# Optimization experiments

Measured on AMD Instinct MI355X. Metric: run time of the kernel, lower is better.

Reference implementation:

```python
import jax, jax.numpy as jnp
import numpy as np

D_MODEL = 1024
N_HEADS = 16
TREE_DEPTH = 5
B, T = 2, 1024


def setup_inputs() -> dict:
    key = jax.random.key(0)
    k1, k2, k3, k4 = jax.random.split(key, 4)
    sc = 1.0 / np.sqrt(D_MODEL)
    return {
        "x": jax.random.normal(k1, (B, T, D_MODEL), dtype=jnp.float32),
        "Wp": jax.random.normal(k2, (D_MODEL, N_HEADS * TREE_DEPTH), dtype=jnp.float32) * sc,
        "bp": jnp.zeros((N_HEADS * TREE_DEPTH,), dtype=jnp.float32),
        "Wv": jax.random.normal(k3, (D_MODEL, D_MODEL), dtype=jnp.float32) * sc,
        "Wo": jax.random.normal(k4, (D_MODEL, D_MODEL), dtype=jnp.float32) * sc,
    }


def reference(x, Wp, bp, Wv, Wo):
    Bc, Tc, d = x.shape
    H, Dt = N_HEADS, TREE_DEPTH
    dh = d // H
    # tree paths: (B, H, T, Dt)
    paths = jax.nn.sigmoid(x @ Wp + bp).reshape(Bc, Tc, H, Dt).transpose(0, 2, 1, 3)
    pq = paths[:, :, :, None, :]  # (B,H,T,1,Dt)
    pk = paths[:, :, None, :, :]  # (B,H,1,T,Dt)
    agree = pq * pk + (1.0 - pq) * (1.0 - pk)  # (B,H,T,T,Dt)
    sim = jnp.cumprod(agree, axis=-1).sum(axis=-1) / Dt  # (B,H,T,T)
    # causal mask (strict upper triangle -> -inf)
    causal_mask = jnp.triu(jnp.ones((Tc, Tc), dtype=bool), k=1)
    sim = jnp.where(causal_mask[None, None], -jnp.inf, sim)
    attn = jax.nn.softmax(sim, axis=-1)
    V = (x @ Wv).reshape(Bc, Tc, H, dh).transpose(0, 2, 1, 3)  # (B,H,T,dh)
    ctx = jnp.einsum("bhqk,bhkd->bhqd", attn, V)
    ctx = ctx.transpose(0, 2, 1, 3).reshape(Bc, Tc, d)
    return ctx @ Wo
```

## Files before the change

kernel.cpp:

```cpp
#include <hip/hip_runtime.h>
#include <hip/hip_bf16.h>

#define B_SZ 2
#define T_SEQ 1024
#define D_MODEL 1024
#define N_HEADS 16
#define TREE_DEPTH 5
#define DH 64

typedef __attribute__((ext_vector_type(8))) short short8;
typedef __attribute__((ext_vector_type(4))) float f32x4;

__device__ __forceinline__ ushort f2bf(float f) {
    uint32_t u = __float_as_uint(f);
    u += 0x7FFFu + ((u >> 16) & 1u);
    return (ushort)(u >> 16);
}

__device__ __forceinline__ void gll16(const void* g, void* l) {
    __builtin_amdgcn_global_load_lds(
        (const __attribute__((address_space(1))) void*)g,
        (__attribute__((address_space(3))) void*)l, 16, 0, 0);
}

__global__ __launch_bounds__(256) void prologue(
    const float* __restrict__ x, const float* __restrict__ Wv,
    const float* __restrict__ Wo, const float* __restrict__ Wp,
    ushort* __restrict__ xb, ushort* __restrict__ Wvt,
    ushort* __restrict__ Wot, ushort* __restrict__ Wpt)
{
    __shared__ __align__(16) char sm[20480];
    const int bid = blockIdx.x, tid = threadIdx.x;
    if (bid < 1024) {
        const int i = (bid * 256 + tid) * 8;
        const float4 a = *(const float4*)(x + i);
        const float4 b = *(const float4*)(x + i + 4);
        ushort o[8] = {f2bf(a.x), f2bf(a.y), f2bf(a.z), f2bf(a.w),
                       f2bf(b.x), f2bf(b.y), f2bf(b.z), f2bf(b.w)};
        *(uint4*)(xb + i) = *(const uint4*)o;
    } else if (bid < 3072) {
        const int t = bid - 1024;
        const float* W = (t < 1024) ? Wv : Wo;
        ushort* Wt = (t < 1024) ? Wvt : Wot;
        const int ti = t & 1023;
        const int n0 = (ti & 31) * 32, k0 = (ti >> 5) * 32;
        float (*tile)[33] = (float(*)[33])sm;
        const int tx = tid & 31, ty = tid >> 5;
        #pragma unroll
        for (int i = 0; i < 4; ++i)
            tile[ty + i * 8][tx] = W[(size_t)(k0 + ty + i * 8) * 1024 + n0 + tx];
        __syncthreads();
        #pragma unroll
        for (int i = 0; i < 4; ++i)
            Wt[(size_t)(n0 + ty + i * 8) * 1024 + k0 + tx] = f2bf(tile[tx][ty + i * 8]);
    } else {
        float* tile = (float*)sm;
        const int k0 = (bid - 3072) * 64;
        #pragma unroll
        for (int j = 0; j < 20; ++j) {
            const int i = tid + j * 256;
            tile[i] = Wp[(size_t)k0 * 80 + i];
        }
        __syncthreads();
        #pragma unroll
        for (int j = 0; j < 20; ++j) {
            const int o = tid + j * 256;
            const int n = o >> 6, k = o & 63;
            Wpt[(size_t)n * 1024 + k0 + k] = f2bf(tile[k * 80 + n]);
        }
    }
}

template <bool OUT_BF16>
__device__ __forceinline__ void gemm_body(
    const ushort* __restrict__ A, const ushort* __restrict__ Bt,
    void* __restrict__ Cv, int N, int K, int bx, int by,
    ushort* As, ushort* Bs)
{
    const int tid = threadIdx.x;
    const int lane = tid & 63;
    const int w = tid >> 6;
    const int wm = w & 1, wn = w >> 1;
    const int rowBase = by * 128;
    const int colBase = bx * 64;

    const int srow = lane & 15;
    const int sk = (lane >> 4) * 8;

    const ushort* gA0 = A + (size_t)(rowBase + 2 * w * 16 + srow) * K + sk;
    const ushort* gA1 = gA0 + (size_t)16 * K;
    const ushort* gB  = Bt + (size_t)(colBase + w * 16 + srow) * K + sk;
    ushort* dA0 = As + (2 * w) * 512;
    ushort* dA1 = As + (2 * w + 1) * 512;
    ushort* dB  = Bs + w * 512;

    f32x4 acc[4][2];
    #pragma unroll
    for (int i = 0; i < 4; ++i) {
        acc[i][0] = (f32x4)0.0f;
        acc[i][1] = (f32x4)0.0f;
    }

    for (int it = 0; it < K / 32; ++it) {
        __syncthreads();
        gll16(gA0 + it * 32, dA0);
        gll16(gA1 + it * 32, dA1);
        gll16(gB  + it * 32, dB);
        __syncthreads();
        short8 af[4], bf[2];
        #pragma unroll
        for (int j = 0; j < 4; ++j)
            af[j] = *(const short8*)(As + (wm * 4 + j) * 512 + lane * 8);
        #pragma unroll
        for (int j = 0; j < 2; ++j)
            bf[j] = *(const short8*)(Bs + (wn * 2 + j) * 512 + lane * 8);
        #pragma unroll
        for (int i = 0; i < 4; ++i)
            #pragma unroll
            for (int j = 0; j < 2; ++j)
                acc[i][j] = __builtin_amdgcn_mfma_f32_16x16x32_bf16(
                    af[i], bf[j], acc[i][j], 0, 0, 0);
    }

    const int cq = lane >> 4, cl = lane & 15;
    #pragma unroll
    for (int i = 0; i < 4; ++i)
        #pragma unroll
        for (int j = 0; j < 2; ++j) {
            const int col = colBase + wn * 32 + j * 16 + cl;
            #pragma unroll
            for (int r = 0; r < 4; ++r) {
                const int row = rowBase + wm * 64 + i * 16 + cq * 4 + r;
                if (OUT_BF16)
                    ((ushort*)Cv)[(size_t)row * N + col] = f2bf(acc[i][j][r]);
                else
                    ((float*)Cv)[(size_t)row * N + col] = acc[i][j][r];
            }
        }
}

__device__ __forceinline__ void phi_body(
    const ushort* __restrict__ xb, const ushort* __restrict__ Wpt,
    const float* __restrict__ bp, ushort* __restrict__ Phi,
    int blk, float* red, float* p_s)
{
    const int tid = threadIdx.x;
    const int lane = tid & 63, w = tid >> 6;
    const int quad = lane >> 4, m16 = lane & 15;
    const int row0 = blk * 16;

    f32x4 acc[5];
    #pragma unroll
    for (int nb = 0; nb < 5; ++nb) acc[nb] = (f32x4)0.0f;

    const ushort* ap = xb + (size_t)(row0 + m16) * 1024 + w * 256 + quad * 8;
    const ushort* bpz = Wpt + (size_t)m16 * 1024 + w * 256 + quad * 8;
    #pragma unroll
    for (int it = 0; it < 8; ++it) {
        const short8 af = *(const short8*)(ap + it * 32);
        #pragma unroll
        for (int nb = 0; nb < 5; ++nb) {
            const short8 bf = *(const short8*)(bpz + (size_t)nb * 16 * 1024 + it * 32);
            acc[nb] = __builtin_amdgcn_mfma_f32_16x16x32_bf16(af, bf, acc[nb], 0, 0, 0);
        }
    }
    #pragma unroll
    for (int nb = 0; nb < 5; ++nb)
        #pragma unroll
        for (int r = 0; r < 4; ++r)
            red[(w * 16 + quad * 4 + r) * 80 + nb * 16 + m16] = acc[nb][r];
    __syncthreads();
    #pragma unroll
    for (int j = 0; j < 5; ++j) {
        const int i = tid + j * 256;
        const int rr = i / 80, cc = i - rr * 80;
        const float v = red[(0 * 16 + rr) * 80 + cc] + red[(1 * 16 + rr) * 80 + cc] +
                        red[(2 * 16 + rr) * 80 + cc] + red[(3 * 16 + rr) * 80 + cc] + bp[cc];
        p_s[rr * 80 + cc] = 1.0f / (1.0f + __expf(-v));
    }
    __syncthreads();
    #pragma unroll
    for (int j = 0; j < 8; ++j) {
        const int c = tid + j * 256;
        const int rr = c >> 7, rem = c & 127;
        const int h = rem >> 3, f8 = (rem & 7) * 8;
        const float* pr = &p_s[rr * 80 + h * 5];
        ushort o[8];
        #pragma unroll
        for (int e = 0; e < 8; ++e) {
            const int f = f8 + e;
            float val = 0.0f;
            if (f < 62) {
                int d, off;
                if (f < 2)       { d = 1; off = 0; }
                else if (f < 6)  { d = 2; off = 2; }
                else if (f < 14) { d = 3; off = 6; }
                else if (f < 30) { d = 4; off = 14; }
                else             { d = 5; off = 30; }
                const int e2 = f - off;
                float prod = 1.0f;
                for (int jj = 1; jj <= d; ++jj) {
                    const float p = pr[jj - 1];
                    prod *= ((e2 >> (d - jj)) & 1) ? (1.0f - p) : p;
                }
                val = prod;
            }
            o[e] = f2bf(val);
        }
        const int grow = row0 + rr;
        const int b = grow >> 10, t = grow & 1023;
        *(uint4*)(Phi + ((size_t)(b * 16 + h) * 1024 + t) * 64 + f8) =
            *(const uint4*)o;
    }
}

__global__ __launch_bounds__(256) void mid_kernel(
    const ushort* __restrict__ xb, const ushort* __restrict__ Wvt,
    const ushort* __restrict__ Wpt, const float* __restrict__ bp,
    ushort* __restrict__ Vt, ushort* __restrict__ Phi)
{
    __shared__ __align__(16) char sm[25600];
    if (blockIdx.x < 256) {
        ushort* As = (ushort*)sm;
        ushort* Bs = As + 128 * 32;
        gemm_body<true>(Wvt, xb, Vt, 2048, 1024,
                        blockIdx.x & 31, blockIdx.x >> 5, As, Bs);
    } else {
        float* red = (float*)sm;
        float* p_s = (float*)(sm + 20480);
        phi_body(xb, Wpt, bp, Phi, blockIdx.x - 256, red, p_s);
    }
}

__global__ __launch_bounds__(256) void gemm_out(
    const ushort* __restrict__ ctxb, const ushort* __restrict__ Wot,
    float* __restrict__ out)
{
    __shared__ __align__(16) ushort sm[128 * 32 + 64 * 32];
    gemm_body<false>(ctxb, Wot, out, 1024, 1024,
                     blockIdx.x, blockIdx.y, sm, sm + 128 * 32);
}

__global__ __launch_bounds__(256) void attn_mfma(
    const ushort* __restrict__ Phi, const ushort* __restrict__ Vt,
    ushort* __restrict__ ctxb)
{
    const int qt = 15 - blockIdx.x;
    const int bh = blockIdx.y;
    const int b = bh >> 4, h = bh & 15;
    const int tid = threadIdx.x;
    const int lane = tid & 63;
    const int w = tid >> 6;
    const int quad = lane >> 4, m16 = lane & 15;

    __shared__ ushort K_s[4096];
    __shared__ ushort V_s[4096];
    __shared__ ushort W_s[4096];

    const int qrow = qt * 64 + w * 16 + m16;
    const ushort* qbase = Phi + ((size_t)bh * 1024 + qrow) * 64 + quad * 8;
    const short8 qf0 = *(const short8*)qbase;
    const short8 qf1 = *(const short8*)(qbase + 32);

    f32x4 cacc[4];
    #pragma unroll
    for (int nb = 0; nb < 4; ++nb) cacc[nb] = (f32x4)0.0f;
    float den[4] = {0.f, 0.f, 0.f, 0.f};

    const int r0 = tid >> 3;
    const int c8 = (tid & 7) * 8;
    const int ks_st = c8 >> 5, kc_st = (c8 >> 3) & 3;

    for (int kt = 0; kt <= qt; ++kt) {
        __syncthreads();
        #pragma unroll
        for (int i = 0; i < 2; ++i) {
            const int r = r0 + i * 32;
            const int dst = ((r >> 4) * 2 + ks_st) * 512 + (kc_st * 16 + (r & 15)) * 8;
            *(uint4*)(K_s + dst) =
                *(const uint4*)(Phi + ((size_t)bh * 1024 + kt * 64 + r) * 64 + c8);
            *(uint4*)(V_s + dst) =
                *(const uint4*)(Vt + (size_t)(h * 64 + r) * (B_SZ * T_SEQ) +
                                b * 1024 + kt * 64 + c8);
        }
        __syncthreads();

        #pragma unroll
        for (int nb = 0; nb < 4; ++nb) {
            const short8 kf0 = *(const short8*)(K_s + (nb * 2 + 0) * 512 + lane * 8);
            const short8 kf1 = *(const short8*)(K_s + (nb * 2 + 1) * 512 + lane * 8);
            f32x4 s = (f32x4)0.0f;
            s = __builtin_amdgcn_mfma_f32_16x16x32_bf16(qf0, kf0, s, 0, 0, 0);
            s = __builtin_amdgcn_mfma_f32_16x16x32_bf16(qf1, kf1, s, 0, 0, 0);
            const int key = nb * 16 + m16;
            const int kglob = kt * 64 + key;
            const int qg0 = qt * 64 + w * 16 + quad * 4;
            const int wbase = (w * 2 + (key >> 5)) * 512 + (((key >> 3) & 3) * 16) * 8 +
                              (quad * 4) * 8 + (key & 7);
            #pragma unroll
            for (int r = 0; r < 4; ++r) {
                float wgt = 0.0f;
                if (kglob <= qg0 + r) wgt = __expf(s[r] * 0.2f);
                den[r] += wgt;
                W_s[wbase + r * 8] = f2bf(wgt);
            }
        }
        __syncthreads();

        const short8 wf0 = *(const short8*)(W_s + (w * 2 + 0) * 512 + lane * 8);
        const short8 wf1 = *(const short8*)(W_s + (w * 2 + 1) * 512 + lane * 8);
        #pragma unroll
        for (int nb = 0; nb < 4; ++nb) {
            const short8 vf0 = *(const short8*)(V_s + (nb * 2 + 0) * 512 + lane * 8);
            const short8 vf1 = *(const short8*)(V_s + (nb * 2 + 1) * 512 + lane * 8);
            cacc[nb] = __builtin_amdgcn_mfma_f32_16x16x32_bf16(wf0, vf0, cacc[nb], 0, 0, 0);
            cacc[nb] = __builtin_amdgcn_mfma_f32_16x16x32_bf16(wf1, vf1, cacc[nb], 0, 0, 0);
        }
    }

    #pragma unroll
    for (int r = 0; r < 4; ++r) {
        den[r] += __shfl_xor(den[r], 1);
        den[r] += __shfl_xor(den[r], 2);
        den[r] += __shfl_xor(den[r], 4);
        den[r] += __shfl_xor(den[r], 8);
        den[r] = 1.0f / den[r];
    }

    #pragma unroll
    for (int nb = 0; nb < 4; ++nb) {
        const int dim = h * 64 + nb * 16 + m16;
        #pragma unroll
        for (int r = 0; r < 4; ++r) {
            const int token = qt * 64 + w * 16 + quad * 4 + r;
            ctxb[(size_t)(b * 1024 + token) * D_MODEL + dim] = f2bf(cacc[nb][r] * den[r]);
        }
    }
}

extern "C" void kernel_launch(void* const* d_in, const int* in_sizes, int n_in,
                              void* d_out, int out_size, void* d_ws, size_t ws_size,
                              hipStream_t stream)
{
    const float* x  = (const float*)d_in[0];
    const float* Wp = (const float*)d_in[1];
    const float* bp = (const float*)d_in[2];
    const float* Wv = (const float*)d_in[3];
    const float* Wo = (const float*)d_in[4];
    float* out = (float*)d_out;

    char* ws = (char*)d_ws;
    ushort* xb   = (ushort*)(ws);
    ushort* Wvt  = (ushort*)(ws + (4u  << 20));
    ushort* Wot  = (ushort*)(ws + (6u  << 20));
    ushort* Phi  = (ushort*)(ws + (8u  << 20));
    ushort* Vt   = (ushort*)(ws + (12u << 20));
    ushort* ctxb = (ushort*)(ws + (16u << 20));
    ushort* Wpt  = (ushort*)(ws + (20u << 20));

    prologue<<<3088, 256, 0, stream>>>(x, Wv, Wo, Wp, xb, Wvt, Wot, Wpt);
    mid_kernel<<<384, 256, 0, stream>>>(xb, Wvt, Wpt, bp, Vt, Phi);
    attn_mfma<<<dim3(16, 32), 256, 0, stream>>>(Phi, Vt, ctxb);
    gemm_out<<<dim3(16, 16), 256, 0, stream>>>(ctxb, Wot, out);
}
```

Before: 160.1 us.

## Double-buffer GEMM and attention tiles with async global-to-LDS loads, shrink GEMM tiles

The shared GEMM body moves from a 128x64 tile with a K-step of 32 to a 64x64 tile with a K-step of 64. It double-buffers LDS so the next tile's global_load_lds is issued before the current tile is computed, and the grids double to 512 blocks for the V projection and 16x32 for the output projection. The attention kernel now streams K and V through double-buffered LDS with async direct-to-LDS loads instead of register staging. It computes transposed scores so each lane packs its weights into one 8-byte LDS write, and reduces the softmax denominator through shared memory. The intent is to hide global load latency, cut barriers per tile and raise occupancy and block count, at the cost of more LDS per block and less reuse per tile.

Result: faster. 151.5 us (-5.4%).

```diff
diff --git a/kernel.cpp b/kernel.cpp
--- a/kernel.cpp
+++ b/kernel.cpp
@@ -81,56 +81,66 @@
     const int lane = tid & 63;
     const int w = tid >> 6;
     const int wm = w & 1, wn = w >> 1;
-    const int rowBase = by * 128;
+    const int rowBase = by * 64;
     const int colBase = bx * 64;
 
     const int srow = lane & 15;
     const int sk = (lane >> 4) * 8;
 
-    const ushort* gA0 = A + (size_t)(rowBase + 2 * w * 16 + srow) * K + sk;
-    const ushort* gA1 = gA0 + (size_t)16 * K;
-    const ushort* gB  = Bt + (size_t)(colBase + w * 16 + srow) * K + sk;
-    ushort* dA0 = As + (2 * w) * 512;
-    ushort* dA1 = As + (2 * w + 1) * 512;
-    ushort* dB  = Bs + w * 512;
-
-    f32x4 acc[4][2];
-    #pragma unroll
-    for (int i = 0; i < 4; ++i) {
+    const ushort* gA = A + (size_t)(rowBase + w * 16 + srow) * K + sk;
+    const ushort* gB = Bt + (size_t)(colBase + w * 16 + srow) * K + sk;
+
+    f32x4 acc[2][2];
+    #pragma unroll
+    for (int i = 0; i < 2; ++i) {
         acc[i][0] = (f32x4)0.0f;
         acc[i][1] = (f32x4)0.0f;
     }
 
-    for (int it = 0; it < K / 32; ++it) {
-        __syncthreads();
-        gll16(gA0 + it * 32, dA0);
-        gll16(gA1 + it * 32, dA1);
-        gll16(gB  + it * 32, dB);
-        __syncthreads();
-        short8 af[4], bf[2];
-        #pragma unroll
-        for (int j = 0; j < 4; ++j)
-            af[j] = *(const short8*)(As + (wm * 4 + j) * 512 + lane * 8);
-        #pragma unroll
-        for (int j = 0; j < 2; ++j)
-            bf[j] = *(const short8*)(Bs + (wn * 2 + j) * 512 + lane * 8);
-        #pragma unroll
-        for (int i = 0; i < 4; ++i)
+    gll16(gA,      As + (w * 2 + 0) * 512);
+    gll16(gA + 32, As + (w * 2 + 1) * 512);
+    gll16(gB,      Bs + (w * 2 + 0) * 512);
+    gll16(gB + 32, Bs + (w * 2 + 1) * 512);
+
+    const int niter = K / 64;
+    for (int it = 0; it < niter; ++it) {
+        __syncthreads();
+        const int cur = (it & 1) * 4096;
+        if (it + 1 < niter) {
+            const int nxt = ((it + 1) & 1) * 4096;
+            const int ko = (it + 1) * 64;
+            gll16(gA + ko,      As + nxt + (w * 2 + 0) * 512);
+            gll16(gA + ko + 32, As + nxt + (w * 2 + 1) * 512);
+            gll16(gB + ko,      Bs + nxt + (w * 2 + 0) * 512);
+            gll16(gB + ko + 32, Bs + nxt + (w * 2 + 1) * 512);
+        }
+        #pragma unroll
+        for (int ks = 0; ks < 2; ++ks) {
+            short8 af[2], bf[2];
+            #pragma unroll
+            for (int i = 0; i < 2; ++i)
+                af[i] = *(const short8*)(As + cur + ((wm * 2 + i) * 2 + ks) * 512 + lane * 8);
             #pragma unroll
             for (int j = 0; j < 2; ++j)
-                acc[i][j] = __builtin_amdgcn_mfma_f32_16x16x32_bf16(
-                    af[i], bf[j], acc[i][j], 0, 0, 0);
-    }
-
-    const int cq = lane >> 4, cl = lane & 15;
-    #pragma unroll
-    for (int i = 0; i < 4; ++i)
+                bf[j] = *(const short8*)(Bs + cur + ((wn * 2 + j) * 2 + ks) * 512 + lane * 8);
+            #pragma unroll
+            for (int i = 0; i < 2; ++i)
+                #pragma unroll
+                for (int j = 0; j < 2; ++j)
+                    acc[i][j] = __builtin_amdgcn_mfma_f32_16x16x32_bf16(
+                        af[i], bf[j], acc[i][j], 0, 0, 0);
+        }
+    }
+
+    const int quad = lane >> 4, m16 = lane & 15;
+    #pragma unroll
+    for (int i = 0; i < 2; ++i)
         #pragma unroll
         for (int j = 0; j < 2; ++j) {
-            const int col = colBase + wn * 32 + j * 16 + cl;
+            const int col = colBase + wn * 32 + j * 16 + m16;
             #pragma unroll
             for (int r = 0; r < 4; ++r) {
-                const int row = rowBase + wm * 64 + i * 16 + cq * 4 + r;
+                const int row = rowBase + wm * 32 + i * 16 + quad * 4 + r;
                 if (OUT_BF16)
                     ((ushort*)Cv)[(size_t)row * N + col] = f2bf(acc[i][j][r]);
                 else
@@ -219,16 +229,16 @@
     const ushort* __restrict__ Wpt, const float* __restrict__ bp,
     ushort* __restrict__ Vt, ushort* __restrict__ Phi)
 {
-    __shared__ __align__(16) char sm[25600];
-    if (blockIdx.x < 256) {
+    __shared__ __align__(16) char sm[32768];
+    if (blockIdx.x < 512) {
         ushort* As = (ushort*)sm;
-        ushort* Bs = As + 128 * 32;
+        ushort* Bs = As + 8192;
         gemm_body<true>(Wvt, xb, Vt, 2048, 1024,
                         blockIdx.x & 31, blockIdx.x >> 5, As, Bs);
     } else {
         float* red = (float*)sm;
         float* p_s = (float*)(sm + 20480);
-        phi_body(xb, Wpt, bp, Phi, blockIdx.x - 256, red, p_s);
+        phi_body(xb, Wpt, bp, Phi, blockIdx.x - 512, red, p_s);
     }
 }
 
@@ -236,9 +246,9 @@
     const ushort* __restrict__ ctxb, const ushort* __restrict__ Wot,
     float* __restrict__ out)
 {
-    __shared__ __align__(16) ushort sm[128 * 32 + 64 * 32];
+    __shared__ __align__(16) ushort sm[16384];
     gemm_body<false>(ctxb, Wot, out, 1024, 1024,
-                     blockIdx.x, blockIdx.y, sm, sm + 128 * 32);
+                     blockIdx.x, blockIdx.y, sm, sm + 8192);
 }
 
 __global__ __launch_bounds__(256) void attn_mfma(
@@ -253,79 +263,83 @@
     const int w = tid >> 6;
     const int quad = lane >> 4, m16 = lane & 15;
 
-    __shared__ ushort K_s[4096];
-    __shared__ ushort V_s[4096];
-    __shared__ ushort W_s[4096];
-
-    const int qrow = qt * 64 + w * 16 + m16;
-    const ushort* qbase = Phi + ((size_t)bh * 1024 + qrow) * 64 + quad * 8;
+    __shared__ __align__(16) ushort K_s[2][4096];
+    __shared__ __align__(16) ushort V_s[2][4096];
+    __shared__ __align__(16) ushort W_s[4096];
+    __shared__ float den_s[4][16];
+
+    const int srow = lane & 15;
+    const int sk = (lane >> 4) * 8;
+    const ushort* gK = Phi + (size_t)bh * 1024 * 64 + (w * 16 + srow) * 64 + sk;
+    const ushort* gV = Vt + (size_t)(h * 64 + w * 16 + srow) * 2048 + b * 1024 + sk;
+
+    const int qglob = qt * 64 + w * 16 + m16;
+    const ushort* qbase = Phi + ((size_t)bh * 1024 + qglob) * 64 + quad * 8;
     const short8 qf0 = *(const short8*)qbase;
     const short8 qf1 = *(const short8*)(qbase + 32);
 
     f32x4 cacc[4];
     #pragma unroll
     for (int nb = 0; nb < 4; ++nb) cacc[nb] = (f32x4)0.0f;
-    float den[4] = {0.f, 0.f, 0.f, 0.f};
-
-    const int r0 = tid >> 3;
-    const int c8 = (tid & 7) * 8;
-    const int ks_st = c8 >> 5, kc_st = (c8 >> 3) & 3;
+    float den = 0.0f;
+
+    gll16(gK,      K_s[0] + (w * 2 + 0) * 512);
+    gll16(gK + 32, K_s[0] + (w * 2 + 1) * 512);
+    gll16(gV,      V_s[0] + (w * 2 + 0) * 512);
+    gll16(gV + 32, V_s[0] + (w * 2 + 1) * 512);
 
     for (int kt = 0; kt <= qt; ++kt) {
-        __syncthreads();
-        #pragma unroll
-        for (int i = 0; i < 2; ++i) {
-            const int r = r0 + i * 32;
-            const int dst = ((r >> 4) * 2 + ks_st) * 512 + (kc_st * 16 + (r & 15)) * 8;
-            *(uint4*)(K_s + dst) =
-                *(const uint4*)(Phi + ((size_t)bh * 1024 + kt * 64 + r) * 64 + c8);
-            *(uint4*)(V_s + dst) =
-                *(const uint4*)(Vt + (size_t)(h * 64 + r) * (B_SZ * T_SEQ) +
-                                b * 1024 + kt * 64 + c8);
-        }
-        __syncthreads();
-
+        const int cur = kt & 1;
+        __syncthreads();
+        if (kt < qt) {
+            const int nxt = cur ^ 1;
+            const ushort* nK = gK + (kt + 1) * 4096;
+            const ushort* nV = gV + (kt + 1) * 64;
+            gll16(nK,      K_s[nxt] + (w * 2 + 0) * 512);
+            gll16(nK + 32, K_s[nxt] + (w * 2 + 1) * 512);
+            gll16(nV,      V_s[nxt] + (w * 2 + 0) * 512);
+            gll16(nV + 32, V_s[nxt] + (w * 2 + 1) * 512);
+        }
         #pragma unroll
         for (int nb = 0; nb < 4; ++nb) {
-            const short8 kf0 = *(const short8*)(K_s + (nb * 2 + 0) * 512 + lane * 8);
-            const short8 kf1 = *(const short8*)(K_s + (nb * 2 + 1) * 512 + lane * 8);
+            const short8 kf0 = *(const short8*)(K_s[cur] + (nb * 2 + 0) * 512 + lane * 8);
+            const short8 kf1 = *(const short8*)(K_s[cur] + (nb * 2 + 1) * 512 + lane * 8);
             f32x4 s = (f32x4)0.0f;
-            s = __builtin_amdgcn_mfma_f32_16x16x32_bf16(qf0, kf0, s, 0, 0, 0);
-            s = __builtin_amdgcn_mfma_f32_16x16x32_bf16(qf1, kf1, s, 0, 0, 0);
-            const int key = nb * 16 + m16;
-            const int kglob = kt * 64 + key;
-            const int qg0 = qt * 64 + w * 16 + quad * 4;
-            const int wbase = (w * 2 + (key >> 5)) * 512 + (((key >> 3) & 3) * 16) * 8 +
-                              (quad * 4) * 8 + (key & 7);
+            s = __builtin_amdgcn_mfma_f32_16x16x32_bf16(kf0, qf0, s, 0, 0, 0);
+            s = __builtin_amdgcn_mfma_f32_16x16x32_bf16(kf1, qf1, s, 0, 0, 0);
+            const int k0g = kt * 64 + nb * 16 + quad * 4;
+            ushort o[4];
             #pragma unroll
             for (int r = 0; r < 4; ++r) {
                 float wgt = 0.0f;
-                if (kglob <= qg0 + r) wgt = __expf(s[r] * 0.2f);
-                den[r] += wgt;
-                W_s[wbase + r * 8] = f2bf(wgt);
+                if (k0g + r <= qglob) wgt = __expf(s[r] * 0.2f);
+                den += wgt;
+                o[r] = f2bf(wgt);
             }
-        }
-        __syncthreads();
-
+            const int addr = (w * 2 + (nb >> 1)) * 512 +
+                             ((nb & 1) * 2 + (quad >> 1)) * 128 +
+                             m16 * 8 + (quad & 1) * 4;
+            *(uint2*)(W_s + addr) = *(const uint2*)o;
+        }
+        __syncthreads();
         const short8 wf0 = *(const short8*)(W_s + (w * 2 + 0) * 512 + lane * 8);
         const short8 wf1 = *(const short8*)(W_s + (w * 2 + 1) * 512 + lane * 8);
         #pragma unroll
         for (int nb = 0; nb < 4; ++nb) {
-            const short8 vf0 = *(const short8*)(V_s + (nb * 2 + 0) * 512 + lane * 8);
-            const short8 vf1 = *(const short8*)(V_s + (nb * 2 + 1) * 512 + lane * 8);
+            const short8 vf0 = *(const short8*)(V_s[cur] + (nb * 2 + 0) * 512 + lane * 8);
+            const short8 vf1 = *(const short8*)(V_s[cur] + (nb * 2 + 1) * 512 + lane * 8);
             cacc[nb] = __builtin_amdgcn_mfma_f32_16x16x32_bf16(wf0, vf0, cacc[nb], 0, 0, 0);
             cacc[nb] = __builtin_amdgcn_mfma_f32_16x16x32_bf16(wf1, vf1, cacc[nb], 0, 0, 0);
         }
     }
 
-    #pragma unroll
-    for (int r = 0; r < 4; ++r) {
-        den[r] += __shfl_xor(den[r], 1);
-        den[r] += __shfl_xor(den[r], 2);
-        den[r] += __shfl_xor(den[r], 4);
-        den[r] += __shfl_xor(den[r], 8);
-        den[r] = 1.0f / den[r];
-    }
+    den += __shfl_xor(den, 16);
+    den += __shfl_xor(den, 32);
+    den_s[w][m16] = den;
+    __syncthreads();
+    float inv[4];
+    #pragma unroll
+    for (int r = 0; r < 4; ++r) inv[r] = 1.0f / den_s[w][quad * 4 + r];
 
     #pragma unroll
     for (int nb = 0; nb < 4; ++nb) {
@@ -333,7 +347,7 @@
         #pragma unroll
         for (int r = 0; r < 4; ++r) {
             const int token = qt * 64 + w * 16 + quad * 4 + r;
-            ctxb[(size_t)(b * 1024 + token) * D_MODEL + dim] = f2bf(cacc[nb][r] * den[r]);
+            ctxb[(size_t)(b * 1024 + token) * D_MODEL + dim] = f2bf(cacc[nb][r] * inv[r]);
         }
     }
 }
@@ -359,7 +373,7 @@
     ushort* Wpt  = (ushort*)(ws + (20u << 20));
 
     prologue<<<3088, 256, 0, stream>>>(x, Wv, Wo, Wp, xb, Wvt, Wot, Wpt);
-    mid_kernel<<<384, 256, 0, stream>>>(xb, Wvt, Wpt, bp, Vt, Phi);
+    mid_kernel<<<640, 256, 0, stream>>>(xb, Wvt, Wpt, bp, Vt, Phi);
     attn_mfma<<<dim3(16, 32), 256, 0, stream>>>(Phi, Vt, ctxb);
-    gemm_out<<<dim3(16, 16), 256, 0, stream>>>(ctxb, Wot, out);
-}
+    gemm_out<<<dim3(16, 32), 256, 0, stream>>>(ctxb, Wot, out);
+}
```
